# Kernel optimization log

Hardware: AMD Instinct MI355X
Metric: run time of the kernel (lower is better)

Reference implementation:

```python
import jax, jax.numpy as jnp
import numpy as np

D_MODEL, D_FFN, N_EXPERTS, TOP_K = 1024, 4096, 8, 2
BATCH, SEQ = 4, 1024


def setup_inputs() -> dict:
    key = jax.random.key(0)
    kx, kr, k1, k2, k3 = jax.random.split(key, 5)
    scale = 0.02
    return {
        "x": jax.random.normal(kx, (BATCH, SEQ, D_MODEL), dtype=jnp.float32),
        "w_router": jax.random.normal(kr, (D_MODEL, N_EXPERTS), dtype=jnp.float32) * scale,
        "w1": jax.random.normal(k1, (N_EXPERTS, D_MODEL, D_FFN), dtype=jnp.float32) * scale,
        "w2": jax.random.normal(k2, (N_EXPERTS, D_FFN, D_MODEL), dtype=jnp.float32) * scale,
        "w3": jax.random.normal(k3, (N_EXPERTS, D_MODEL, D_FFN), dtype=jnp.float32) * scale,
    }


def reference(x, w_router, w1, w2, w3):
    B, S, D = x.shape
    E = w_router.shape[1]
    T = B * S
    xf = x.reshape(T, D)

    # --- router: softmax over experts, top-k, renormalize ---
    router_probs = jax.nn.softmax(xf @ w_router, axis=-1)          # (T, E)
    topk_probs, topk_idx = jax.lax.top_k(router_probs, TOP_K)      # (T, K)
    topk_probs = topk_probs / topk_probs.sum(axis=-1, keepdims=True)

    # per-token combine weight for each expert (top_k indices are distinct,
    # matching the torch per-slot accumulation exactly)
    comb = jnp.zeros((T, E), dtype=xf.dtype)
    comb = comb.at[jnp.arange(T)[:, None], topk_idx].add(topk_probs)  # (T, E)

    # --- dense SwiGLU experts (same math as masked loop) ---
    h = jnp.einsum("td,edf->tef", xf, w1)                          # (T, E, F)
    g = jnp.einsum("td,edf->tef", xf, w3)                          # (T, E, F)
    y = jnp.einsum("tef,efd->ted", jax.nn.silu(h) * g, w2)         # (T, E, D)
    out = jnp.einsum("te,ted->td", comb, y).reshape(B, S, D)

    # --- load-balance aux loss ---
    expert_mask = jax.nn.one_hot(topk_idx, E, dtype=jnp.float32).sum(axis=1)  # (T, E)
    tokens_per_expert = expert_mask.sum(axis=0) / T
    mean_probs = router_probs.mean(axis=0)
    aux_loss = E * jnp.sum(tokens_per_expert * mean_probs)
    return out, aux_loss
```

## Files before the change

### kernel.cpp

```cpp
#include <hip/hip_runtime.h>
#include <hip/hip_bf16.h>
#include <cstdint>
#include <cstddef>

#define TT 4096
#define DM 1024
#define DF 4096
#define NE 8
#define BTAB 72
#define BTAB2 40

typedef __attribute__((ext_vector_type(8))) short bf16x8;
typedef __attribute__((ext_vector_type(8))) unsigned short ushort8;
typedef __attribute__((ext_vector_type(4))) float f32x4;

static __device__ __forceinline__ unsigned short f2bf(float f) {
    union { float f; unsigned int u; } v; v.f = f;
    unsigned int u = v.u;
    return (unsigned short)((u + 0x7FFFu + ((u >> 16) & 1u)) >> 16);
}
static __device__ __forceinline__ float bf2f(unsigned short h) {
    union { unsigned int u; float f; } v; v.u = ((unsigned int)h) << 16;
    return v.f;
}

#define GLOAD16(gsrc, ldst)                                                        \
    __builtin_amdgcn_global_load_lds(                                              \
        (const __attribute__((address_space(1))) void*)(gsrc),                     \
        (__attribute__((address_space(3))) void*)(ldst), 16, 0, 0)

__global__ void transpose_v2(const float* __restrict__ in,
                             unsigned short* __restrict__ out,
                             int R, int C) {
    __shared__ float tile[64][65];
    const int e = blockIdx.z;
    const float* src = in + (size_t)e * R * C;
    unsigned short* dst = out + (size_t)e * R * C;
    const int c0 = blockIdx.x * 64, r0 = blockIdx.y * 64;
    const int tid = threadIdx.x;
    #pragma unroll
    for (int i = 0; i < 4; ++i) {
        int idx = tid + i * 256;
        int rr = idx >> 4, cc = idx & 15;
        float4 v = *(const float4*)(src + (size_t)(r0 + rr) * C + c0 + cc * 4);
        tile[rr][cc * 4 + 0] = v.x;
        tile[rr][cc * 4 + 1] = v.y;
        tile[rr][cc * 4 + 2] = v.z;
        tile[rr][cc * 4 + 3] = v.w;
    }
    __syncthreads();
    #pragma unroll
    for (int i = 0; i < 2; ++i) {
        int idx = tid + i * 256;
        int c = idx >> 3, rc = idx & 7;
        ushort8 o;
        #pragma unroll
        for (int j = 0; j < 8; ++j) o[j] = f2bf(tile[rc * 8 + j][c]);
        *(ushort8*)(dst + (size_t)(c0 + c) * R + r0 + rc * 8) = o;
    }
}

__global__ void router_kernel(const float* __restrict__ x,
                              const float* __restrict__ wr,
                              unsigned short* __restrict__ xb,
                              int* __restrict__ topi, float* __restrict__ topw,
                              float* __restrict__ probsum) {
    __shared__ float s_ps[NE];
    const int tid = threadIdx.x;
    if (tid < NE) s_ps[tid] = 0.f;
    __syncthreads();
    const int wid = tid >> 6, lane = tid & 63;
    const int t = blockIdx.x * 4 + wid;
    float acc[NE] = {0.f, 0.f, 0.f, 0.f, 0.f, 0.f, 0.f, 0.f};
    const float* xr = x + (size_t)t * DM;
    unsigned short* xbr = xb + (size_t)t * DM;
    for (int it = 0; it < DM / 64; ++it) {
        int d = it * 64 + lane;
        float xv = xr[d];
        xbr[d] = f2bf(xv);
        const float* w = wr + d * NE;
        #pragma unroll
        for (int e = 0; e < NE; ++e) acc[e] = fmaf(xv, w[e], acc[e]);
    }
    #pragma unroll
    for (int e = 0; e < NE; ++e) {
        float v = acc[e];
        #pragma unroll
        for (int off = 32; off; off >>= 1) v += __shfl_xor(v, off);
        acc[e] = v;
    }
    if (lane == 0) {
        float m = acc[0];
        #pragma unroll
        for (int e = 1; e < NE; ++e) m = fmaxf(m, acc[e]);
        float p[NE], s = 0.f;
        #pragma unroll
        for (int e = 0; e < NE; ++e) { p[e] = expf(acc[e] - m); s += p[e]; }
        float inv = 1.f / s;
        #pragma unroll
        for (int e = 0; e < NE; ++e) { p[e] *= inv; atomicAdd(&s_ps[e], p[e]); }
        int i1 = 0; float p1 = p[0];
        #pragma unroll
        for (int e = 1; e < NE; ++e) if (p[e] > p1) { p1 = p[e]; i1 = e; }
        int i2 = -1; float p2 = -1.f;
        #pragma unroll
        for (int e = 0; e < NE; ++e) if (e != i1 && p[e] > p2) { p2 = p[e]; i2 = e; }
        float rs = 1.f / (p1 + p2);
        topi[t * 2] = i1; topi[t * 2 + 1] = i2;
        topw[t * 2] = p1 * rs; topw[t * 2 + 1] = p2 * rs;
    }
    __syncthreads();
    if (tid < NE) atomicAdd(&probsum[tid], s_ps[tid]);
}

__global__ void assign_kernel(const int* __restrict__ topi,
                              int* __restrict__ list, int* __restrict__ slotpos,
                              int* __restrict__ cnt) {
    const int e = blockIdx.x;
    __shared__ int s_wc[4];
    const int tid = threadIdx.x, wid = tid >> 6, lane = tid & 63;
    int running = 0;
    for (int base = 0; base < TT; base += 256) {
        int t = base + tid;
        int hit = 0, slot = 0;
        int a = topi[2 * t], b = topi[2 * t + 1];
        if (a == e) { hit = 1; slot = 0; }
        else if (b == e) { hit = 1; slot = 1; }
        unsigned long long m = __ballot(hit);
        if (lane == 0) s_wc[wid] = __popcll(m);
        __syncthreads();
        int pre = 0, tot = 0;
        #pragma unroll
        for (int q = 0; q < 4; ++q) { int c = s_wc[q]; tot += c; if (q < wid) pre += c; }
        if (hit) {
            int pos = running + pre + __popcll(m & ((1ull << lane) - 1ull));
            list[e * TT + pos] = t;
            slotpos[2 * t + slot] = pos;
        }
        running += tot;
        __syncthreads();
    }
    if (tid == 0) cnt[e] = running;
}

__global__ void finalize_kernel(const int* __restrict__ cnt,
                                const float* __restrict__ probsum,
                                int* __restrict__ offs,
                                unsigned int* __restrict__ blocktab,
                                unsigned int* __restrict__ blocktab2,
                                float* __restrict__ out_aux) {
    int o = 0;
    float aux = 0.f;
    int nb = 0, nb2 = 0;
    for (int e = 0; e < NE; ++e) {
        offs[e] = o; o += cnt[e];
        aux += (float)cnt[e] * probsum[e];
        int nrb = (cnt[e] + 127) >> 7;
        for (int rb = 0; rb < nrb; ++rb) blocktab[nb++] = ((unsigned)e << 16) | rb;
        int nrb2 = (cnt[e] + 255) >> 8;
        for (int rb = 0; rb < nrb2; ++rb) blocktab2[nb2++] = ((unsigned)e << 16) | rb;
    }
    while (nb < BTAB) blocktab[nb++] = 0xFFFFFFFFu;
    while (nb2 < BTAB2) blocktab2[nb2++] = 0xFFFFFFFFu;
    *out_aux = (float)NE * aux / ((float)TT * (float)TT);
}

__global__ __launch_bounds__(512, 2) void gemm1_kernel(
    const unsigned short* __restrict__ xb,
    const unsigned short* __restrict__ w1T,
    const unsigned short* __restrict__ w3T,
    unsigned short* __restrict__ act,
    const int* __restrict__ list,
    const int* __restrict__ cnt,
    const int* __restrict__ offs,
    const unsigned int* __restrict__ blocktab2) {
    const int lin = blockIdx.y * 32 + blockIdx.x;
    const int xcd = lin & 7, j = lin >> 3;
    const int fcolb = xcd * 4 + (j & 3);
    const int slot = j >> 2;
    const unsigned int tab = blocktab2[slot];
    if (tab == 0xFFFFFFFFu) return;
    const int e = tab >> 16;
    const int rowbase = (int)(tab & 0xFFFFu) << 8;
    const int ce = cnt[e];
    const int fbase = fcolb * 128;

    __shared__ __align__(16) unsigned short lds[65536];
    char* ldsC = (char*)lds;

    const int tid = threadIdx.x;
    const int lane = tid & 63, wid = tid >> 6;
    const int wm = wid >> 2, wn = wid & 3;

    const unsigned short* aP[2][2];
    const unsigned short* bP[2][2];
    #pragma unroll
    for (int ci = 0; ci < 2; ++ci) {
        const int c = tid + ci * 512;
        const int r = (c >> 2) & 15, rg = c >> 7, cc = c & 3, ks = (c >> 6) & 1;
        const int row = rg * 16 + r;
        const int kb = ks * 64 + ((cc * 16) ^ ((r & 8) << 2));
        #pragma unroll
        for (int h = 0; h < 2; ++h) {
            int sp = rowbase + h * 128 + row; if (sp >= ce) sp = ce - 1;
            aP[h][ci] = xb + (size_t)list[e * TT + sp] * DM + (kb >> 1);
            const int n = h * 128 + row;
            const int col = fbase + (n >> 5) * 16 + (n & 15);
            const unsigned short* wsrc = ((n >> 4) & 1) ? w3T : w1T;
            bP[h][ci] = wsrc + ((size_t)e * DF + col) * DM + (kb >> 1);
        }
    }

#define STG_A(H, T, B) {                                                          \
    GLOAD16(aP[H][0] + (size_t)(T) * 64, ldsC + (B) * 65536 + (H) * 16384 + tid * 16);        \
    GLOAD16(aP[H][1] + (size_t)(T) * 64, ldsC + (B) * 65536 + (H) * 16384 + 8192 + tid * 16); }
#define STG_B(H, T, B) {                                                          \
    GLOAD16(bP[H][0] + (size_t)(T) * 64, ldsC + (B) * 65536 + 32768 + (H) * 16384 + tid * 16);        \
    GLOAD16(bP[H][1] + (size_t)(T) * 64, ldsC + (B) * 65536 + 32768 + (H) * 16384 + 8192 + tid * 16); }

    const int lofs = ((lane & 15) << 6) + ((((lane >> 4) << 4) ^ ((lane & 8) << 2)));

#define RDA(BB, MQ) { _Pragma("unroll") for (int i = 0; i < 4; ++i) {             \
    _Pragma("unroll") for (int k2 = 0; k2 < 2; ++k2)                              \
        aq[i][k2] = *(const bf16x8*)(ldsC + (BB) + wm * 16384 +                   \
                     (((MQ) * 4 + i) * 2 + k2) * 1024 + lofs); } }
#define RDB(DST, BB, NQ) { _Pragma("unroll") for (int u = 0; u < 2; ++u) {        \
    _Pragma("unroll") for (int k2 = 0; k2 < 2; ++k2)                              \
        DST[u][k2] = *(const bf16x8*)(ldsC + (BB) + 32768 + (wn >> 1) * 16384 +   \
                     (wn & 1) * 8192 + ((NQ) * 2 + u) * 2048 + k2 * 1024 + lofs); } }
#define MMQ(MQ, NQ, BQ) { __builtin_amdgcn_s_setprio(1);                          \
    _Pragma("unroll") for (int i = 0; i < 4; ++i)                                 \
    _Pragma("unroll") for (int u = 0; u < 2; ++u)                                 \
    _Pragma("unroll") for (int k2 = 0; k2 < 2; ++k2)                              \
        acc[(MQ) * 4 + i][(NQ) * 2 + u] = __builtin_amdgcn_mfma_f32_16x16x32_bf16(\
            aq[i][k2], BQ[u][k2], acc[(MQ) * 4 + i][(NQ) * 2 + u], 0, 0, 0);      \
    __builtin_amdgcn_s_setprio(0); }

    f32x4 acc[8][4] = {};
    bf16x8 aq[4][2], b0[2][2], b1[2][2];

    STG_A(0, 0, 0); STG_A(1, 0, 0); STG_B(0, 0, 0); STG_B(1, 0, 0);
    STG_B(0, 1, 1); STG_B(1, 1, 1); STG_A(0, 1, 1);
    asm volatile("s_waitcnt vmcnt(6)" ::: "memory");
    __builtin_amdgcn_s_barrier();

    #pragma unroll 1
    for (int h = 0; h < 16; ++h) {
        const int bb = (h & 1) * 65536;
        RDA(bb, 0) RDB(b0, bb, 0)
        if (h < 15) STG_A(1, h + 1, (h & 1) ^ 1);
        __builtin_amdgcn_s_barrier();
        __builtin_amdgcn_sched_barrier(0);
        MMQ(0, 0, b0)
        __builtin_amdgcn_sched_barrier(0);
        __builtin_amdgcn_s_barrier();
        RDB(b1, bb, 1)
        __builtin_amdgcn_s_barrier();
        __builtin_amdgcn_sched_barrier(0);
        MMQ(0, 1, b1)
        __builtin_amdgcn_sched_barrier(0);
        __builtin_amdgcn_s_barrier();
        RDA(bb, 1)
        if (h < 14) STG_B(0, h + 2, h & 1);
        __builtin_amdgcn_s_barrier();
        __builtin_amdgcn_sched_barrier(0);
        MMQ(1, 0, b0)
        __builtin_amdgcn_sched_barrier(0);
        __builtin_amdgcn_s_barrier();
        if (h < 14) { STG_B(1, h + 2, h & 1); STG_A(0, h + 2, h & 1); }
        __builtin_amdgcn_s_barrier();
        __builtin_amdgcn_sched_barrier(0);
        MMQ(1, 1, b1)
        __builtin_amdgcn_sched_barrier(0);
        if (h < 14)       { asm volatile("s_waitcnt vmcnt(6)" ::: "memory"); }
        else if (h == 14) { asm volatile("s_waitcnt vmcnt(0)" ::: "memory"); }
        __builtin_amdgcn_s_barrier();
    }
#undef STG_A
#undef STG_B
#undef RDA
#undef RDB
#undef MMQ

    const int ob = offs[e];
    const int g = lane >> 4, rr = lane & 15;
    #pragma unroll
    for (int m = 0; m < 8; ++m) {
        #pragma unroll
        for (int j2 = 0; j2 < 4; ++j2) {
            const int pos = rowbase + wm * 128 + m * 16 + g * 4 + j2;
            if (pos < ce) {
                unsigned short* arow = act + (size_t)(ob + pos) * DF + fbase + wn * 32;
                #pragma unroll
                for (int p = 0; p < 2; ++p) {
                    float hv = acc[m][2 * p][j2];
                    float gv = acc[m][2 * p + 1][j2];
                    float a = (hv / (1.f + __expf(-hv))) * gv;
                    arow[p * 16 + rr] = f2bf(a);
                }
            }
        }
    }
}

static __device__ __forceinline__ const bf16x8* frag_ptr(
        const unsigned short* base, int row, int ph16) {
    return (const bf16x8*)((const char*)base + row * 64 + ph16);
}

__global__ __launch_bounds__(256, 3) void gemm2_kernel(
    const unsigned short* __restrict__ act,
    const unsigned short* __restrict__ w2T,
    unsigned short* __restrict__ ybuf,
    const int* __restrict__ cnt,
    const int* __restrict__ offs,
    const unsigned int* __restrict__ blocktab) {
    const int lin = blockIdx.y * 8 + blockIdx.x;
    const int dcolb = lin & 7;
    const int slot = lin >> 3;
    const unsigned int tab = blocktab[slot];
    if (tab == 0xFFFFFFFFu) return;
    const int e = tab >> 16;
    const int rowbase = (int)(tab & 0xFFFFu) << 7;
    const int ce = cnt[e];
    const int dbase = dcolb * 128;
    const int ob = offs[e];

    __shared__ __align__(16) unsigned short As[3 * 128 * 32];
    __shared__ __align__(16) unsigned short Bs[3 * 128 * 32];

    const int tid = threadIdx.x;
    const int lrow = tid >> 2;
    const int q = (tid & 3) ^ ((tid >> 3) & 3);

    int sp0 = rowbase + lrow;       if (sp0 >= ce) sp0 = ce - 1;
    int sp1 = rowbase + 64 + lrow;  if (sp1 >= ce) sp1 = ce - 1;

    const unsigned short* a0 = act + (size_t)(ob + sp0) * DF + q * 8;
    const unsigned short* a1 = act + (size_t)(ob + sp1) * DF + q * 8;
    const unsigned short* b0 = w2T + ((size_t)e * DM + dbase + lrow) * DF + q * 8;
    const unsigned short* b1 = b0 + (size_t)64 * DF;

    char* ldsA = (char*)As + tid * 16;
    char* ldsB = (char*)Bs + tid * 16;

    const int wid = tid >> 6, lane = tid & 63;
    const int wm = wid >> 1, wn = wid & 1;
    const int g = lane >> 4, r = lane & 15;
    const int ph16 = (g ^ ((r >> 1) & 3)) << 4;

    f32x4 acc[4][4] = {};

#define STAGE2(T, BUF)                                   \
    {   const int koff = (T) * 32;                       \
        const int bo = (BUF) * 8192;                     \
        GLOAD16(a0 + koff, ldsA + bo);                   \
        GLOAD16(a1 + koff, ldsA + bo + 4096);            \
        GLOAD16(b0 + koff, ldsB + bo);                   \
        GLOAD16(b1 + koff, ldsB + bo + 4096); }

#define COMP2(BS)                                                           \
    {   const unsigned short* Ac = As + (BS) * 4096;                        \
        const unsigned short* Bc = Bs + (BS) * 4096;                        \
        bf16x8 af[4];                                                       \
        _Pragma("unroll") for (int m = 0; m < 4; ++m)                       \
            af[m] = *frag_ptr(Ac, wm * 64 + m * 16 + r, ph16);              \
        _Pragma("unroll") for (int n = 0; n < 4; ++n) {                     \
            bf16x8 bfr = *frag_ptr(Bc, wn * 64 + n * 16 + r, ph16);         \
            _Pragma("unroll") for (int m = 0; m < 4; ++m)                   \
                acc[m][n] = __builtin_amdgcn_mfma_f32_16x16x32_bf16(af[m], bfr, acc[m][n], 0, 0, 0); } }

    const int NT = DF / 32;
    STAGE2(0, 0);
    STAGE2(1, 1);
    int bs = 0, sb = 2;
    for (int t = 0; t < NT - 2; ++t) {
        STAGE2(t + 2, sb);
        asm volatile("s_waitcnt vmcnt(8)" ::: "memory");
        __builtin_amdgcn_s_barrier();
        COMP2(bs)
        asm volatile("" ::: "memory");
        __builtin_amdgcn_s_barrier();
        bs = (bs + 1 == 3) ? 0 : bs + 1;
        sb = (sb + 1 == 3) ? 0 : sb + 1;
    }
    asm volatile("s_waitcnt vmcnt(4)" ::: "memory");
    __builtin_amdgcn_s_barrier();
    COMP2(bs)
    asm volatile("" ::: "memory");
    __builtin_amdgcn_s_barrier();
    bs = (bs + 1 == 3) ? 0 : bs + 1;
    asm volatile("s_waitcnt vmcnt(0)" ::: "memory");
    __builtin_amdgcn_s_barrier();
    COMP2(bs)
#undef STAGE2
#undef COMP2

    #pragma unroll
    for (int m = 0; m < 4; ++m) {
        #pragma unroll
        for (int j2 = 0; j2 < 4; ++j2) {
            const int pos = rowbase + wm * 64 + m * 16 + g * 4 + j2;
            if (pos < ce) {
                unsigned short* yrow = ybuf + (size_t)(ob + pos) * DM + dbase + wn * 64;
                #pragma unroll
                for (int n = 0; n < 4; ++n)
                    yrow[n * 16 + r] = f2bf(acc[m][n][j2]);
            }
        }
    }
}

__global__ void combine_kernel(const unsigned short* __restrict__ ybuf,
                               const int* __restrict__ topi,
                               const float* __restrict__ topw,
                               const int* __restrict__ slotpos,
                               const int* __restrict__ offs,
                               float* __restrict__ out) {
    const int t = blockIdx.x;
    const int tid = threadIdx.x;
    const int e0 = topi[2 * t], e1 = topi[2 * t + 1];
    const int r0 = offs[e0] + slotpos[2 * t];
    const int r1 = offs[e1] + slotpos[2 * t + 1];
    const float w0 = topw[2 * t], w1 = topw[2 * t + 1];
    ushort4 a = *(const ushort4*)(ybuf + (size_t)r0 * DM + tid * 4);
    ushort4 b = *(const ushort4*)(ybuf + (size_t)r1 * DM + tid * 4);
    float4 o;
    o.x = w0 * bf2f(a.x) + w1 * bf2f(b.x);
    o.y = w0 * bf2f(a.y) + w1 * bf2f(b.y);
    o.z = w0 * bf2f(a.z) + w1 * bf2f(b.z);
    o.w = w0 * bf2f(a.w) + w1 * bf2f(b.w);
    *(float4*)(out + (size_t)t * DM + tid * 4) = o;
}

extern "C" void kernel_launch(void* const* d_in, const int* in_sizes, int n_in,
                              void* d_out, int out_size, void* d_ws, size_t ws_size,
                              hipStream_t stream) {
    (void)in_sizes; (void)n_in; (void)ws_size;
    const float* x  = (const float*)d_in[0];
    const float* wr = (const float*)d_in[1];
    const float* w1 = (const float*)d_in[2];
    const float* w2 = (const float*)d_in[3];
    const float* w3 = (const float*)d_in[4];
    float* out = (float*)d_out;

    char* ws = (char*)d_ws;
    size_t off = 0;
    auto alloc = [&](size_t bytes) -> void* {
        void* p = ws + off;
        off = (off + bytes + 255) & ~(size_t)255;
        return p;
    };
    unsigned short* w1T = (unsigned short*)alloc((size_t)NE * DF * DM * 2);
    unsigned short* w3T = (unsigned short*)alloc((size_t)NE * DF * DM * 2);
    unsigned short* w2T = (unsigned short*)alloc((size_t)NE * DM * DF * 2);
    unsigned short* act = (unsigned short*)alloc((size_t)2 * TT * DF * 2);
    unsigned short* xb  = (unsigned short*)alloc((size_t)TT * DM * 2);
    int*   topi    = (int*)alloc(TT * 2 * sizeof(int));
    float* topw    = (float*)alloc(TT * 2 * sizeof(float));
    int*   list    = (int*)alloc((size_t)NE * TT * sizeof(int));
    int*   slotpos = (int*)alloc(TT * 2 * sizeof(int));
    int*   cnt     = (int*)alloc(NE * sizeof(int));
    int*   offs    = (int*)alloc(NE * sizeof(int));
    float* probsum = (float*)alloc(NE * sizeof(float));
    unsigned int* blocktab  = (unsigned int*)alloc(BTAB * sizeof(unsigned int));
    unsigned int* blocktab2 = (unsigned int*)alloc(BTAB2 * sizeof(unsigned int));
    unsigned short* ybuf = w1T;

    hipMemsetAsync(probsum, 0, NE * sizeof(float), stream);

    dim3 tb(256);
    transpose_v2<<<dim3(DF / 64, DM / 64, NE), tb, 0, stream>>>(w1, w1T, DM, DF);
    transpose_v2<<<dim3(DF / 64, DM / 64, NE), tb, 0, stream>>>(w3, w3T, DM, DF);
    transpose_v2<<<dim3(DM / 64, DF / 64, NE), tb, 0, stream>>>(w2, w2T, DF, DM);

    router_kernel<<<TT / 4, 256, 0, stream>>>(x, wr, xb, topi, topw, probsum);
    assign_kernel<<<NE, 256, 0, stream>>>(topi, list, slotpos, cnt);
    finalize_kernel<<<1, 1, 0, stream>>>(cnt, probsum, offs, blocktab, blocktab2, out + (out_size - 1));

    gemm1_kernel<<<dim3(32, BTAB2), 512, 0, stream>>>(xb, w1T, w3T, act, list, cnt, offs, blocktab2);
    gemm2_kernel<<<dim3(8, BTAB), 256, 0, stream>>>(act, w2T, ybuf, cnt, offs, blocktab);
    combine_kernel<<<TT, 256, 0, stream>>>(ybuf, topi, topw, slotpos, offs, out);
}
```

Baseline: 445.8 us.

## Retile expert down-projection GEMM to 256x128 with 8-wave double-buffered pipeline

The second expert GEMM moves from a 128x128 tile with 256 threads and a 3-stage BK=32 ring to a 256x128 tile with 512 threads. It uses BK=64 double buffering, swizzled LDS fragments, and the same quarter-interleaved load/MFMA schedule as the first GEMM, indexed by the 256-row block table. The larger tile is meant to raise reuse of each w2 column block and cut redundant weight traffic. In the first GEMM, several intra-iteration barriers and sched_barriers are removed and the launch bound is relaxed to one block per CU. This trades some occupancy and scheduling control for fewer stalls, and it risks LDS races if the dropped barriers were needed.

```diff
diff --git a/kernel.cpp b/kernel.cpp
--- a/kernel.cpp
+++ b/kernel.cpp
@@ -165,7 +165,7 @@
     *out_aux = (float)NE * aux / ((float)TT * (float)TT);
 }
 
-__global__ __launch_bounds__(512, 2) void gemm1_kernel(
+__global__ __launch_bounds__(512, 1) void gemm1_kernel(
     const unsigned short* __restrict__ xb,
     const unsigned short* __restrict__ w1T,
     const unsigned short* __restrict__ w3T,
@@ -249,29 +249,17 @@
         const int bb = (h & 1) * 65536;
         RDA(bb, 0) RDB(b0, bb, 0)
         if (h < 15) STG_A(1, h + 1, (h & 1) ^ 1);
-        __builtin_amdgcn_s_barrier();
-        __builtin_amdgcn_sched_barrier(0);
         MMQ(0, 0, b0)
-        __builtin_amdgcn_sched_barrier(0);
         __builtin_amdgcn_s_barrier();
         RDB(b1, bb, 1)
-        __builtin_amdgcn_s_barrier();
-        __builtin_amdgcn_sched_barrier(0);
         MMQ(0, 1, b1)
-        __builtin_amdgcn_sched_barrier(0);
         __builtin_amdgcn_s_barrier();
         RDA(bb, 1)
         if (h < 14) STG_B(0, h + 2, h & 1);
-        __builtin_amdgcn_s_barrier();
-        __builtin_amdgcn_sched_barrier(0);
         MMQ(1, 0, b0)
-        __builtin_amdgcn_sched_barrier(0);
         __builtin_amdgcn_s_barrier();
         if (h < 14) { STG_B(1, h + 2, h & 1); STG_A(0, h + 2, h & 1); }
-        __builtin_amdgcn_s_barrier();
-        __builtin_amdgcn_sched_barrier(0);
         MMQ(1, 1, b1)
-        __builtin_amdgcn_sched_barrier(0);
         if (h < 14)       { asm volatile("s_waitcnt vmcnt(6)" ::: "memory"); }
         else if (h == 14) { asm volatile("s_waitcnt vmcnt(0)" ::: "memory"); }
         __builtin_amdgcn_s_barrier();
@@ -303,99 +291,105 @@
     }
 }
 
-static __device__ __forceinline__ const bf16x8* frag_ptr(
-        const unsigned short* base, int row, int ph16) {
-    return (const bf16x8*)((const char*)base + row * 64 + ph16);
-}
-
-__global__ __launch_bounds__(256, 3) void gemm2_kernel(
+__global__ __launch_bounds__(512, 1) void gemm2_kernel(
     const unsigned short* __restrict__ act,
     const unsigned short* __restrict__ w2T,
     unsigned short* __restrict__ ybuf,
     const int* __restrict__ cnt,
     const int* __restrict__ offs,
-    const unsigned int* __restrict__ blocktab) {
-    const int lin = blockIdx.y * 8 + blockIdx.x;
-    const int dcolb = lin & 7;
-    const int slot = lin >> 3;
-    const unsigned int tab = blocktab[slot];
+    const unsigned int* __restrict__ blocktab2) {
+    const unsigned int tab = blocktab2[blockIdx.y];
     if (tab == 0xFFFFFFFFu) return;
     const int e = tab >> 16;
-    const int rowbase = (int)(tab & 0xFFFFu) << 7;
+    const int rowbase = (int)(tab & 0xFFFFu) << 8;
     const int ce = cnt[e];
-    const int dbase = dcolb * 128;
     const int ob = offs[e];
-
-    __shared__ __align__(16) unsigned short As[3 * 128 * 32];
-    __shared__ __align__(16) unsigned short Bs[3 * 128 * 32];
+    const int dbase = blockIdx.x * 128;
+
+    __shared__ __align__(16) unsigned short lds[49152];
+    char* ldsC = (char*)lds;
 
     const int tid = threadIdx.x;
-    const int lrow = tid >> 2;
-    const int q = (tid & 3) ^ ((tid >> 3) & 3);
-
-    int sp0 = rowbase + lrow;       if (sp0 >= ce) sp0 = ce - 1;
-    int sp1 = rowbase + 64 + lrow;  if (sp1 >= ce) sp1 = ce - 1;
-
-    const unsigned short* a0 = act + (size_t)(ob + sp0) * DF + q * 8;
-    const unsigned short* a1 = act + (size_t)(ob + sp1) * DF + q * 8;
-    const unsigned short* b0 = w2T + ((size_t)e * DM + dbase + lrow) * DF + q * 8;
-    const unsigned short* b1 = b0 + (size_t)64 * DF;
-
-    char* ldsA = (char*)As + tid * 16;
-    char* ldsB = (char*)Bs + tid * 16;
-
-    const int wid = tid >> 6, lane = tid & 63;
+    const int lane = tid & 63, wid = tid >> 6;
     const int wm = wid >> 1, wn = wid & 1;
-    const int g = lane >> 4, r = lane & 15;
-    const int ph16 = (g ^ ((r >> 1) & 3)) << 4;
+
+    const unsigned short* aP[2][2];
+    const unsigned short* bP[2];
+    #pragma unroll
+    for (int ci = 0; ci < 2; ++ci) {
+        const int c = tid + ci * 512;
+        const int r = (c >> 2) & 15, rg = c >> 7, cc = c & 3, ks = (c >> 6) & 1;
+        const int row = rg * 16 + r;
+        const int kb = ks * 64 + ((cc * 16) ^ ((r & 8) << 2));
+        #pragma unroll
+        for (int h = 0; h < 2; ++h) {
+            int sp = rowbase + h * 128 + row; if (sp >= ce) sp = ce - 1;
+            aP[h][ci] = act + (size_t)(ob + sp) * DF + (kb >> 1);
+        }
+        bP[ci] = w2T + ((size_t)e * DM + dbase + row) * DF + (kb >> 1);
+    }
+
+#define STG2_A(H, T, B) {                                                         \
+    GLOAD16(aP[H][0] + (size_t)(T) * 64, ldsC + (B) * 49152 + (H) * 16384 + tid * 16);        \
+    GLOAD16(aP[H][1] + (size_t)(T) * 64, ldsC + (B) * 49152 + (H) * 16384 + 8192 + tid * 16); }
+#define STG2_B(T, B) {                                                            \
+    GLOAD16(bP[0] + (size_t)(T) * 64, ldsC + (B) * 49152 + 32768 + tid * 16);     \
+    GLOAD16(bP[1] + (size_t)(T) * 64, ldsC + (B) * 49152 + 32768 + 8192 + tid * 16); }
+
+    const int lofs = ((lane & 15) << 6) + ((((lane >> 4) << 4) ^ ((lane & 8) << 2)));
+
+#define RD2A(BB, MQ) { _Pragma("unroll") for (int i = 0; i < 2; ++i) {            \
+    _Pragma("unroll") for (int k2 = 0; k2 < 2; ++k2)                              \
+        aq[i][k2] = *(const bf16x8*)(ldsC + (BB) + (wm >> 1) * 16384 +            \
+                     (((wm & 1) * 4 + (MQ) * 2 + i) * 2 + k2) * 1024 + lofs); } }
+#define RD2B(DST, BB, NQ) { _Pragma("unroll") for (int u = 0; u < 2; ++u) {       \
+    _Pragma("unroll") for (int k2 = 0; k2 < 2; ++k2)                              \
+        DST[u][k2] = *(const bf16x8*)(ldsC + (BB) + 32768 +                       \
+                     ((wn * 4 + (NQ) * 2 + u) * 2 + k2) * 1024 + lofs); } }
+#define MMQ2(MQ, NQ, BQ) { __builtin_amdgcn_s_setprio(1);                         \
+    _Pragma("unroll") for (int i = 0; i < 2; ++i)                                 \
+    _Pragma("unroll") for (int u = 0; u < 2; ++u)                                 \
+    _Pragma("unroll") for (int k2 = 0; k2 < 2; ++k2)                              \
+        acc[(MQ) * 2 + i][(NQ) * 2 + u] = __builtin_amdgcn_mfma_f32_16x16x32_bf16(\
+            aq[i][k2], BQ[u][k2], acc[(MQ) * 2 + i][(NQ) * 2 + u], 0, 0, 0);      \
+    __builtin_amdgcn_s_setprio(0); }
 
     f32x4 acc[4][4] = {};
-
-#define STAGE2(T, BUF)                                   \
-    {   const int koff = (T) * 32;                       \
-        const int bo = (BUF) * 8192;                     \
-        GLOAD16(a0 + koff, ldsA + bo);                   \
-        GLOAD16(a1 + koff, ldsA + bo + 4096);            \
-        GLOAD16(b0 + koff, ldsB + bo);                   \
-        GLOAD16(b1 + koff, ldsB + bo + 4096); }
-
-#define COMP2(BS)                                                           \
-    {   const unsigned short* Ac = As + (BS) * 4096;                        \
-        const unsigned short* Bc = Bs + (BS) * 4096;                        \
-        bf16x8 af[4];                                                       \
-        _Pragma("unroll") for (int m = 0; m < 4; ++m)                       \
-            af[m] = *frag_ptr(Ac, wm * 64 + m * 16 + r, ph16);              \
-        _Pragma("unroll") for (int n = 0; n < 4; ++n) {                     \
-            bf16x8 bfr = *frag_ptr(Bc, wn * 64 + n * 16 + r, ph16);         \
-            _Pragma("unroll") for (int m = 0; m < 4; ++m)                   \
-                acc[m][n] = __builtin_amdgcn_mfma_f32_16x16x32_bf16(af[m], bfr, acc[m][n], 0, 0, 0); } }
-
-    const int NT = DF / 32;
-    STAGE2(0, 0);
-    STAGE2(1, 1);
-    int bs = 0, sb = 2;
-    for (int t = 0; t < NT - 2; ++t) {
-        STAGE2(t + 2, sb);
-        asm volatile("s_waitcnt vmcnt(8)" ::: "memory");
-        __builtin_amdgcn_s_barrier();
-        COMP2(bs)
-        asm volatile("" ::: "memory");
-        __builtin_amdgcn_s_barrier();
-        bs = (bs + 1 == 3) ? 0 : bs + 1;
-        sb = (sb + 1 == 3) ? 0 : sb + 1;
-    }
+    bf16x8 aq[2][2], b0[2][2], b1[2][2];
+
+    const int NT = DF / 64;
+    STG2_A(0, 0, 0); STG2_A(1, 0, 0); STG2_B(0, 0);
+    STG2_B(1, 1); STG2_A(0, 1, 1);
     asm volatile("s_waitcnt vmcnt(4)" ::: "memory");
     __builtin_amdgcn_s_barrier();
-    COMP2(bs)
-    asm volatile("" ::: "memory");
-    __builtin_amdgcn_s_barrier();
-    bs = (bs + 1 == 3) ? 0 : bs + 1;
-    asm volatile("s_waitcnt vmcnt(0)" ::: "memory");
-    __builtin_amdgcn_s_barrier();
-    COMP2(bs)
-#undef STAGE2
-#undef COMP2
-
+
+    #pragma unroll 1
+    for (int h = 0; h < NT; ++h) {
+        const int bb = (h & 1) * 49152;
+        RD2A(bb, 0) RD2B(b0, bb, 0)
+        if (h + 1 < NT) STG2_A(1, h + 1, (h & 1) ^ 1);
+        MMQ2(0, 0, b0)
+        __builtin_amdgcn_s_barrier();
+        RD2B(b1, bb, 1)
+        MMQ2(0, 1, b1)
+        __builtin_amdgcn_s_barrier();
+        RD2A(bb, 1)
+        if (h + 2 < NT) STG2_B(h + 2, h & 1);
+        MMQ2(1, 0, b0)
+        __builtin_amdgcn_s_barrier();
+        if (h + 2 < NT) STG2_A(0, h + 2, h & 1);
+        MMQ2(1, 1, b1)
+        if (h + 2 < NT)      { asm volatile("s_waitcnt vmcnt(4)" ::: "memory"); }
+        else if (h + 1 < NT) { asm volatile("s_waitcnt vmcnt(0)" ::: "memory"); }
+        __builtin_amdgcn_s_barrier();
+    }
+#undef STG2_A
+#undef STG2_B
+#undef RD2A
+#undef RD2B
+#undef MMQ2
+
+    const int g = lane >> 4, rr = lane & 15;
     #pragma unroll
     for (int m = 0; m < 4; ++m) {
         #pragma unroll
@@ -405,7 +399,7 @@
                 unsigned short* yrow = ybuf + (size_t)(ob + pos) * DM + dbase + wn * 64;
                 #pragma unroll
                 for (int n = 0; n < 4; ++n)
-                    yrow[n * 16 + r] = f2bf(acc[m][n][j2]);
+                    yrow[n * 16 + rr] = f2bf(acc[m][n][j2]);
             }
         }
     }
@@ -479,6 +473,6 @@
     finalize_kernel<<<1, 1, 0, stream>>>(cnt, probsum, offs, blocktab, blocktab2, out + (out_size - 1));
 
     gemm1_kernel<<<dim3(32, BTAB2), 512, 0, stream>>>(xb, w1T, w3T, act, list, cnt, offs, blocktab2);
-    gemm2_kernel<<<dim3(8, BTAB), 256, 0, stream>>>(act, w2T, ybuf, cnt, offs, blocktab);
+    gemm2_kernel<<<dim3(8, BTAB2), 512, 0, stream>>>(act, w2T, ybuf, cnt, offs, blocktab2);
     combine_kernel<<<TT, 256, 0, stream>>>(ybuf, topi, topw, slotpos, offs, out);
 }
```

Result: no change. 440.4 us (-1.2%).
